# Kernel optimization log

Hardware: AMD Instinct MI355X
Metric: run time of the kernel (lower is better)

## Reference

```python
import jax, jax.numpy as jnp
import numpy as np

IN_C = 64
OUT_C = 64
NUM_RELS = 32
N_NODES = 20000
N_EDGES = 50000


def setup_inputs() -> dict:
    key = jax.random.key(0)
    k1, k2, k3, k4, k5, k6, k7 = jax.random.split(key, 7)
    x = jax.random.normal(k1, (N_NODES, IN_C), dtype=jnp.float32)
    edge_index = jax.random.randint(k2, (2, N_EDGES), 0, N_NODES, dtype=jnp.int64)
    edge_type = jax.random.randint(k3, (N_EDGES,), 0, NUM_RELS, dtype=jnp.int64)
    weight_fwd = jax.random.normal(k4, (NUM_RELS, IN_C * OUT_C), dtype=jnp.float32)
    weight_bwd = jax.random.normal(k5, (NUM_RELS, IN_C * OUT_C), dtype=jnp.float32)
    lin_w = jax.random.normal(k6, (OUT_C, IN_C), dtype=jnp.float32) * (1.0 / np.sqrt(IN_C))
    lin_b = jax.random.normal(k7, (OUT_C,), dtype=jnp.float32) * 0.01
    return {"x": x, "edge_index": edge_index, "edge_type": edge_type,
            "weight_fwd": weight_fwd, "weight_bwd": weight_bwd,
            "lin_w": lin_w, "lin_b": lin_b}


def type_gcn_conv(x, src, dst, edge_type, weight_table):
    # degrees[e] = (# edges sharing src[e]) + 1  (faithful to pairwise-compare count)
    n_nodes = x.shape[0]
    counts = jax.ops.segment_sum(jnp.ones(src.shape[0], jnp.float32), src,
                                 num_segments=n_nodes)
    degrees = counts[src] + 1.0                      # [E]
    w = weight_table[edge_type]                      # [E, in*out] gather
    w = w / (jnp.linalg.norm(w, axis=1, keepdims=True) + 0.01)
    w = w / degrees[:, None]
    w = w.reshape(-1, IN_C, OUT_C)                   # [E, in, out]
    msg = jnp.einsum('ei,eio->eo', x[src], w)        # per-edge small matmul
    return jax.ops.segment_sum(msg, dst, num_segments=n_nodes)  # scatter-add at dst


def reference(x, edge_index, edge_type, weight_fwd, weight_bwd, lin_w, lin_b):
    src, dst = edge_index[0], edge_index[1]
    fwd = type_gcn_conv(x, src, dst, edge_type, weight_fwd)
    # backward conv sees reversed edge_index: its src is original dst
    bwd = type_gcn_conv(x, dst, src, edge_type, weight_bwd)
    return x @ lin_w.T + lin_b + fwd + bwd
```

## Files before the change

kernel.cpp:

```cpp
#include <hip/hip_runtime.h>

#define NREL 32

typedef short short8 __attribute__((ext_vector_type(8)));
typedef float f32x4 __attribute__((ext_vector_type(4)));

__device__ inline unsigned short f2bf(float f) {
    union { float f; unsigned u; } u; u.f = f;
    unsigned r = u.u + 0x7FFF + ((u.u >> 16) & 1);
    return (unsigned short)(r >> 16);
}


__global__ void count_kernel(const int* __restrict__ src, const int* __restrict__ dst,
                             const int* __restrict__ et,
                             float* __restrict__ cntf, float* __restrict__ cntb,
                             int* __restrict__ hist, int E) {
    __shared__ int lh[NREL];
    if (threadIdx.x < NREL) lh[threadIdx.x] = 0;
    __syncthreads();
    int e = blockIdx.x * blockDim.x + threadIdx.x;
    if (e < E) {
        atomicAdd(&cntf[src[e]], 1.0f);
        atomicAdd(&cntb[dst[e]], 1.0f);
        atomicAdd(&lh[et[e]], 1);
    }
    __syncthreads();
    if (threadIdx.x < NREL && lh[threadIdx.x]) atomicAdd(&hist[threadIdx.x], lh[threadIdx.x]);
}

__global__ void norm_kernel(const float* __restrict__ wf, const float* __restrict__ wb,
                            unsigned short* __restrict__ wtb) {
    int rel = blockIdx.x & 31;
    int tab = blockIdx.x >> 5;
    const float* s_ = (tab ? wb : wf) + rel * 4096;
    unsigned short* d_ = wtb + (size_t)blockIdx.x * 4096;
    int tid = threadIdx.x;

    float ssum = 0.f;
    #pragma unroll
    for (int k = 0; k < 16; k += 4) {
        float4 v = *(const float4*)(s_ + tid * 16 + k);
        ssum += v.x * v.x + v.y * v.y + v.z * v.z + v.w * v.w;
    }
    #pragma unroll
    for (int off = 32; off >= 1; off >>= 1) ssum += __shfl_down(ssum, off, 64);

    __shared__ float part[4];
    __shared__ float scale_s;
    if ((tid & 63) == 0) part[tid >> 6] = ssum;
    __syncthreads();
    if (tid == 0) scale_s = 1.0f / (sqrtf(part[0] + part[1] + part[2] + part[3]) + 0.01f);
    __syncthreads();
    float sc = scale_s;
    int i = tid >> 2, o0 = (tid & 3) * 16;
    #pragma unroll
    for (int q = 0; q < 4; ++q) {
        float4 v = *(const float4*)(s_ + i * 64 + o0 + q * 4);
        d_[(o0 + q * 4 + 0) * 64 + i] = f2bf(v.x * sc);
        d_[(o0 + q * 4 + 1) * 64 + i] = f2bf(v.y * sc);
        d_[(o0 + q * 4 + 2) * 64 + i] = f2bf(v.z * sc);
        d_[(o0 + q * 4 + 3) * 64 + i] = f2bf(v.w * sc);
    }
}

__global__ void prefix_kernel(const int* __restrict__ hist, int* __restrict__ bstart,
                              int* __restrict__ cinfo, int maxC) {
    __shared__ int off[NREL + 1];
    int tid = threadIdx.x;
    if (tid == 0) {
        int acc = 0;
        for (int b = 0; b < NREL; ++b) {
            off[b] = acc;
            bstart[b] = acc;
            acc += ((hist[b] + 63) >> 6) << 6;
        }
        off[NREL] = acc;
    }
    __syncthreads();
    for (int c = tid; c < maxC; c += blockDim.x) {
        int pos = c * 64;
        if (pos >= off[NREL]) { cinfo[c] = -1; continue; }
        int lo = 0, hi = NREL;
        while (hi - lo > 1) { int mid = (lo + hi) >> 1; if (off[mid] <= pos) lo = mid; else hi = mid; }
        cinfo[c] = lo;
    }
}

__global__ void scatter_kernel(const int* __restrict__ et, int* __restrict__ fill,
                               const int* __restrict__ bstart, int* __restrict__ sorted, int E) {
    __shared__ int lh[NREL];
    __shared__ int lbase[NREL];
    int tid = threadIdx.x;
    if (tid < NREL) lh[tid] = 0;
    __syncthreads();
    int e = blockIdx.x * blockDim.x + tid;
    int r = 0, my = 0;
    bool valid = (e < E);
    if (valid) { r = et[e]; my = atomicAdd(&lh[r], 1); }
    __syncthreads();
    if (tid < NREL && lh[tid]) lbase[tid] = atomicAdd(&fill[tid], lh[tid]);
    __syncthreads();
    if (valid) sorted[bstart[r] + lbase[r] + my] = e;
}

__global__ void transpose_lw(const float* __restrict__ lw, float* __restrict__ lwT) {
    int t = threadIdx.x;
    for (int k = t * 16; k < t * 16 + 16; ++k) {
        int o = k & 63, i = k >> 6;
        lwT[k] = lw[o * 64 + i];
    }
}

__global__ void linear_kernel(const float* __restrict__ x, const float* __restrict__ lwT,
                              const float* __restrict__ lb, float* __restrict__ out, int N) {
    __shared__ float xs[4][64];
    int lane = threadIdx.x & 63;
    int wslot = threadIdx.x >> 6;
    int n = blockIdx.x * 4 + wslot;
    bool valid = (n < N);
    int nn = valid ? n : 0;
    xs[wslot][lane] = x[nn * 64 + lane];
    __syncthreads();
    float acc = lb[lane];
    #pragma unroll
    for (int i = 0; i < 64; i += 4) {
        float4 xi = *(const float4*)(&xs[wslot][i]);
        acc = fmaf(xi.x, lwT[(i + 0) * 64 + lane], acc);
        acc = fmaf(xi.y, lwT[(i + 1) * 64 + lane], acc);
        acc = fmaf(xi.z, lwT[(i + 2) * 64 + lane], acc);
        acc = fmaf(xi.w, lwT[(i + 3) * 64 + lane], acc);
    }
    if (valid) out[n * 64 + lane] = acc;
}

#define APITCH 72
__global__ __launch_bounds__(256) void conv_mfma(
        const float* __restrict__ x,
        const int* __restrict__ src, const int* __restrict__ dst,
        const float* __restrict__ cntf, const float* __restrict__ cntb,
        const unsigned short* __restrict__ wtb,
        const int* __restrict__ cinfo, const int* __restrict__ sorted,
        float* __restrict__ out) {
    int rel = cinfo[blockIdx.x];
    if (rel < 0) return;
    int dir = blockIdx.y;

    __shared__ unsigned short As[64 * APITCH];
    __shared__ unsigned short Bs[64 * APITCH];
    __shared__ int dstS[64];

    int tid = threadIdx.x;
    int j = tid >> 2, part = tid & 3;

    {
        const uint4* s4 = (const uint4*)(wtb + (size_t)((dir << 5) + rel) * 4096 + j * 64 + part * 16);
        uint4 v0 = s4[0], v1 = s4[1];
        *(uint4*)(&Bs[j * APITCH + part * 16]) = v0;
        *(uint4*)(&Bs[j * APITCH + part * 16 + 8]) = v1;
    }

    int e = sorted[blockIdx.x * 64 + j];
    if (e < 0) {
        uint4 z = {0, 0, 0, 0};
        *(uint4*)(&As[j * APITCH + part * 16]) = z;
        *(uint4*)(&As[j * APITCH + part * 16 + 8]) = z;
        if (part == 0) dstS[j] = -1;
    } else {
        int s_ = dir ? dst[e] : src[e];
        int d_ = dir ? src[e] : dst[e];
        float cv = dir ? cntb[s_] : cntf[s_];
        float inv = 1.0f / (cv + 1.0f);
        const float4* xr = (const float4*)(x + (size_t)s_ * 64 + part * 16);
        float4 v0 = xr[0], v1 = xr[1], v2 = xr[2], v3 = xr[3];
        uint4 r0, r1;
        r0.x = f2bf(v0.x * inv) | ((unsigned)f2bf(v0.y * inv) << 16);
        r0.y = f2bf(v0.z * inv) | ((unsigned)f2bf(v0.w * inv) << 16);
        r0.z = f2bf(v1.x * inv) | ((unsigned)f2bf(v1.y * inv) << 16);
        r0.w = f2bf(v1.z * inv) | ((unsigned)f2bf(v1.w * inv) << 16);
        r1.x = f2bf(v2.x * inv) | ((unsigned)f2bf(v2.y * inv) << 16);
        r1.y = f2bf(v2.z * inv) | ((unsigned)f2bf(v2.w * inv) << 16);
        r1.z = f2bf(v3.x * inv) | ((unsigned)f2bf(v3.y * inv) << 16);
        r1.w = f2bf(v3.z * inv) | ((unsigned)f2bf(v3.w * inv) << 16);
        *(uint4*)(&As[j * APITCH + part * 16]) = r0;
        *(uint4*)(&As[j * APITCH + part * 16 + 8]) = r1;
        if (part == 0) dstS[j] = d_;
    }
    __syncthreads();

    int lane = tid & 63, w = tid >> 6;
    int m = lane & 15, quad = lane >> 4;
    f32x4 acc0 = {0.f, 0.f, 0.f, 0.f}, acc1 = acc0, acc2 = acc0, acc3 = acc0;
    #pragma unroll
    for (int k0 = 0; k0 < 64; k0 += 32) {
        short8 a  = *(const short8*)(&As[(w * 16 + m) * APITCH + k0 + quad * 8]);
        short8 b0 = *(const short8*)(&Bs[(0  + m) * APITCH + k0 + quad * 8]);
        short8 b1 = *(const short8*)(&Bs[(16 + m) * APITCH + k0 + quad * 8]);
        short8 b2 = *(const short8*)(&Bs[(32 + m) * APITCH + k0 + quad * 8]);
        short8 b3 = *(const short8*)(&Bs[(48 + m) * APITCH + k0 + quad * 8]);
        acc0 = __builtin_amdgcn_mfma_f32_16x16x32_bf16(a, b0, acc0, 0, 0, 0);
        acc1 = __builtin_amdgcn_mfma_f32_16x16x32_bf16(a, b1, acc1, 0, 0, 0);
        acc2 = __builtin_amdgcn_mfma_f32_16x16x32_bf16(a, b2, acc2, 0, 0, 0);
        acc3 = __builtin_amdgcn_mfma_f32_16x16x32_bf16(a, b3, acc3, 0, 0, 0);
    }

    int row_base = w * 16 + quad * 4;
    #pragma unroll
    for (int r = 0; r < 4; ++r) {
        int d_ = dstS[row_base + r];
        if (d_ >= 0) {
            float* op = out + (size_t)d_ * 64 + m;
            atomicAdd(op +  0, acc0[r]);
            atomicAdd(op + 16, acc1[r]);
            atomicAdd(op + 32, acc2[r]);
            atomicAdd(op + 48, acc3[r]);
        }
    }
}

extern "C" void kernel_launch(void* const* d_in, const int* in_sizes, int n_in,
                              void* d_out, int out_size, void* d_ws, size_t ws_size,
                              hipStream_t stream) {
    const float* x  = (const float*)d_in[0];
    const int*   ei = (const int*)  d_in[1];
    const int*   et = (const int*)  d_in[2];
    const float* wf = (const float*)d_in[3];
    const float* wb = (const float*)d_in[4];
    const float* lw = (const float*)d_in[5];
    const float* lb = (const float*)d_in[6];
    float* out = (float*)d_out;

    const int E = in_sizes[2];
    const int N = in_sizes[0] / 64;
    const int maxC = ((E + 63) >> 6) + NREL;

    char* p = (char*)d_ws;
    unsigned short* wtb = (unsigned short*)p;  p += (size_t)2 * NREL * 4096 * sizeof(unsigned short);
    float* lwT  = (float*)p;                   p += 4096 * sizeof(float);
    float* cntf = (float*)p;                   p += (size_t)N * sizeof(float);
    float* cntb = (float*)p;                   p += (size_t)N * sizeof(float);
    int*   hist = (int*)p;                     p += NREL * sizeof(int);
    int*   fill = (int*)p;                     p += NREL * sizeof(int);
    int*   bst  = (int*)p;                     p += NREL * sizeof(int);
    int*   cinfo = (int*)p;                    p += (size_t)maxC * sizeof(int);
    int*   sorted = (int*)p;                   p += (size_t)maxC * 64 * sizeof(int);

    const int* srcp = ei;
    const int* dstp = ei + E;

    hipMemsetAsync(cntf, 0, ((size_t)2 * N + 2 * NREL) * sizeof(float), stream);
    hipMemsetAsync(sorted, 0xFF, (size_t)maxC * 64 * sizeof(int), stream);

    count_kernel<<<(E + 255) / 256, 256, 0, stream>>>(srcp, dstp, et, cntf, cntb, hist, E);
    prefix_kernel<<<1, 256, 0, stream>>>(hist, bst, cinfo, maxC);
    scatter_kernel<<<(E + 255) / 256, 256, 0, stream>>>(et, fill, bst, sorted, E);
    norm_kernel<<<64, 256, 0, stream>>>(wf, wb, wtb);
    transpose_lw<<<1, 256, 0, stream>>>(lw, lwT);
    linear_kernel<<<(N + 3) / 4, 256, 0, stream>>>(x, lwT, lb, out, N);
    dim3 cgrid(maxC, 2);
    conv_mfma<<<cgrid, 256, 0, stream>>>(x, srcp, dstp, cntf, cntb, wtb, cinfo, sorted, out);
}
```

Baseline: 134.9 us.

## Fuse setup kernels into one launch and derive bucket offsets on the fly

Measured after the change: 115.2 us. 14.6% less time.

```diff
diff --git a/kernel.cpp b/kernel.cpp
--- a/kernel.cpp
+++ b/kernel.cpp
@@ -11,87 +11,122 @@
     return (unsigned short)(r >> 16);
 }
 
-
-__global__ void count_kernel(const int* __restrict__ src, const int* __restrict__ dst,
-                             const int* __restrict__ et,
-                             float* __restrict__ cntf, float* __restrict__ cntb,
-                             int* __restrict__ hist, int E) {
-    __shared__ int lh[NREL];
-    if (threadIdx.x < NREL) lh[threadIdx.x] = 0;
-    __syncthreads();
-    int e = blockIdx.x * blockDim.x + threadIdx.x;
-    if (e < E) {
-        atomicAdd(&cntf[src[e]], 1.0f);
-        atomicAdd(&cntb[dst[e]], 1.0f);
-        atomicAdd(&lh[et[e]], 1);
-    }
-    __syncthreads();
-    if (threadIdx.x < NREL && lh[threadIdx.x]) atomicAdd(&hist[threadIdx.x], lh[threadIdx.x]);
-}
-
-__global__ void norm_kernel(const float* __restrict__ wf, const float* __restrict__ wb,
-                            unsigned short* __restrict__ wtb) {
-    int rel = blockIdx.x & 31;
-    int tab = blockIdx.x >> 5;
-    const float* s_ = (tab ? wb : wf) + rel * 4096;
-    unsigned short* d_ = wtb + (size_t)blockIdx.x * 4096;
+__device__ inline void bucket_scan(const int* __restrict__ hist, int lane,
+                                   int& h, int& P, int& excl) {
+    h = (lane < NREL) ? hist[lane] : 0;
+    P = ((h + 63) >> 6) << 6;
+    int s = P;
+    #pragma unroll
+    for (int off = 1; off < 32; off <<= 1) {
+        int t = __shfl_up(s, off, 64);
+        if ((lane & 31) >= off) s += t;
+    }
+    excl = s - P;
+}
+
+
+__global__ __launch_bounds__(256) void setup_kernel(
+        const float* __restrict__ x,
+        const int* __restrict__ src, const int* __restrict__ dst,
+        const int* __restrict__ et,
+        const float* __restrict__ wf, const float* __restrict__ wb,
+        const float* __restrict__ lw, const float* __restrict__ lb,
+        float* __restrict__ cntf, float* __restrict__ cntb,
+        int* __restrict__ hist, unsigned short* __restrict__ wtb,
+        float* __restrict__ out, int E, int N, int nCountB) {
+    __shared__ float smem[4 * 8 * 64 + 8];
     int tid = threadIdx.x;
-
-    float ssum = 0.f;
-    #pragma unroll
-    for (int k = 0; k < 16; k += 4) {
-        float4 v = *(const float4*)(s_ + tid * 16 + k);
-        ssum += v.x * v.x + v.y * v.y + v.z * v.z + v.w * v.w;
-    }
-    #pragma unroll
-    for (int off = 32; off >= 1; off >>= 1) ssum += __shfl_down(ssum, off, 64);
-
-    __shared__ float part[4];
-    __shared__ float scale_s;
-    if ((tid & 63) == 0) part[tid >> 6] = ssum;
-    __syncthreads();
-    if (tid == 0) scale_s = 1.0f / (sqrtf(part[0] + part[1] + part[2] + part[3]) + 0.01f);
-    __syncthreads();
-    float sc = scale_s;
-    int i = tid >> 2, o0 = (tid & 3) * 16;
-    #pragma unroll
-    for (int q = 0; q < 4; ++q) {
-        float4 v = *(const float4*)(s_ + i * 64 + o0 + q * 4);
-        d_[(o0 + q * 4 + 0) * 64 + i] = f2bf(v.x * sc);
-        d_[(o0 + q * 4 + 1) * 64 + i] = f2bf(v.y * sc);
-        d_[(o0 + q * 4 + 2) * 64 + i] = f2bf(v.z * sc);
-        d_[(o0 + q * 4 + 3) * 64 + i] = f2bf(v.w * sc);
-    }
-}
-
-__global__ void prefix_kernel(const int* __restrict__ hist, int* __restrict__ bstart,
-                              int* __restrict__ cinfo, int maxC) {
-    __shared__ int off[NREL + 1];
-    int tid = threadIdx.x;
-    if (tid == 0) {
-        int acc = 0;
-        for (int b = 0; b < NREL; ++b) {
-            off[b] = acc;
-            bstart[b] = acc;
-            acc += ((hist[b] + 63) >> 6) << 6;
-        }
-        off[NREL] = acc;
-    }
-    __syncthreads();
-    for (int c = tid; c < maxC; c += blockDim.x) {
-        int pos = c * 64;
-        if (pos >= off[NREL]) { cinfo[c] = -1; continue; }
-        int lo = 0, hi = NREL;
-        while (hi - lo > 1) { int mid = (lo + hi) >> 1; if (off[mid] <= pos) lo = mid; else hi = mid; }
-        cinfo[c] = lo;
+    int b = blockIdx.x;
+
+    if (b < nCountB) {
+        int* lh = (int*)smem;
+        if (tid < NREL) lh[tid] = 0;
+        __syncthreads();
+        int e = b * 256 + tid;
+        if (e < E) {
+            atomicAdd(&cntf[src[e]], 1.0f);
+            atomicAdd(&cntb[dst[e]], 1.0f);
+            atomicAdd(&lh[et[e]], 1);
+        }
+        __syncthreads();
+        if (tid < NREL && lh[tid]) atomicAdd(&hist[tid], lh[tid]);
+        return;
+    }
+    b -= nCountB;
+    if (b < 64) {
+        int rel = b & 31, tab = b >> 5;
+        const float* s_ = (tab ? wb : wf) + rel * 4096;
+        unsigned short* d_ = wtb + (size_t)b * 4096;
+        float* part = smem;
+        float ssum = 0.f;
+        #pragma unroll
+        for (int k = 0; k < 16; k += 4) {
+            float4 v = *(const float4*)(s_ + tid * 16 + k);
+            ssum += v.x * v.x + v.y * v.y + v.z * v.z + v.w * v.w;
+        }
+        #pragma unroll
+        for (int off = 32; off >= 1; off >>= 1) ssum += __shfl_down(ssum, off, 64);
+        if ((tid & 63) == 0) part[tid >> 6] = ssum;
+        __syncthreads();
+        if (tid == 0) part[4] = 1.0f / (sqrtf(part[0] + part[1] + part[2] + part[3]) + 0.01f);
+        __syncthreads();
+        float sc = part[4];
+        int i = tid >> 2, o0 = (tid & 3) * 16;
+        #pragma unroll
+        for (int q = 0; q < 4; ++q) {
+            float4 v = *(const float4*)(s_ + i * 64 + o0 + q * 4);
+            d_[(o0 + q * 4 + 0) * 64 + i] = f2bf(v.x * sc);
+            d_[(o0 + q * 4 + 1) * 64 + i] = f2bf(v.y * sc);
+            d_[(o0 + q * 4 + 2) * 64 + i] = f2bf(v.z * sc);
+            d_[(o0 + q * 4 + 3) * 64 + i] = f2bf(v.w * sc);
+        }
+        return;
+    }
+    b -= 64;
+    {
+        int lane = tid & 63, w = tid >> 6;
+        int nodeBase = b * 32 + w * 8;
+        float4 wrow[16];
+        const float4* lwrow = (const float4*)(lw + lane * 64);
+        #pragma unroll
+        for (int g = 0; g < 16; ++g) wrow[g] = lwrow[g];
+        float bias = lb[lane];
+        float* xs = smem + w * 8 * 64;
+        #pragma unroll
+        for (int t = 0; t < 8; ++t) {
+            int n = nodeBase + t;
+            if (n < N) xs[t * 64 + lane] = x[(size_t)n * 64 + lane];
+        }
+        __syncthreads();
+        for (int t = 0; t < 8; ++t) {
+            int n = nodeBase + t;
+            if (n >= N) break;
+            float acc = bias;
+            const float4* xr = (const float4*)(xs + t * 64);
+            #pragma unroll
+            for (int g = 0; g < 16; ++g) {
+                float4 xv = xr[g];
+                acc = fmaf(xv.x, wrow[g].x, acc);
+                acc = fmaf(xv.y, wrow[g].y, acc);
+                acc = fmaf(xv.z, wrow[g].z, acc);
+                acc = fmaf(xv.w, wrow[g].w, acc);
+            }
+            out[(size_t)n * 64 + lane] = acc;
+        }
     }
 }
 
 __global__ void scatter_kernel(const int* __restrict__ et, int* __restrict__ fill,
-                               const int* __restrict__ bstart, int* __restrict__ sorted, int E) {
+                               const int* __restrict__ hist, int* __restrict__ sorted, int E) {
     __shared__ int lh[NREL];
     __shared__ int lbase[NREL];
+    __shared__ int bstartS[NREL];
     int tid = threadIdx.x;
+    if (tid < 64) {
+        int h, P, excl;
+        bucket_scan(hist, tid, h, P, excl);
+        if (tid < NREL) bstartS[tid] = excl;
+    }
     if (tid < NREL) lh[tid] = 0;
     __syncthreads();
     int e = blockIdx.x * blockDim.x + tid;
@@ -101,37 +136,7 @@
     __syncthreads();
     if (tid < NREL && lh[tid]) lbase[tid] = atomicAdd(&fill[tid], lh[tid]);
     __syncthreads();
-    if (valid) sorted[bstart[r] + lbase[r] + my] = e;
-}
-
-__global__ void transpose_lw(const float* __restrict__ lw, float* __restrict__ lwT) {
-    int t = threadIdx.x;
-    for (int k = t * 16; k < t * 16 + 16; ++k) {
-        int o = k & 63, i = k >> 6;
-        lwT[k] = lw[o * 64 + i];
-    }
-}
-
-__global__ void linear_kernel(const float* __restrict__ x, const float* __restrict__ lwT,
-                              const float* __restrict__ lb, float* __restrict__ out, int N) {
-    __shared__ float xs[4][64];
-    int lane = threadIdx.x & 63;
-    int wslot = threadIdx.x >> 6;
-    int n = blockIdx.x * 4 + wslot;
-    bool valid = (n < N);
-    int nn = valid ? n : 0;
-    xs[wslot][lane] = x[nn * 64 + lane];
-    __syncthreads();
-    float acc = lb[lane];
-    #pragma unroll
-    for (int i = 0; i < 64; i += 4) {
-        float4 xi = *(const float4*)(&xs[wslot][i]);
-        acc = fmaf(xi.x, lwT[(i + 0) * 64 + lane], acc);
-        acc = fmaf(xi.y, lwT[(i + 1) * 64 + lane], acc);
-        acc = fmaf(xi.z, lwT[(i + 2) * 64 + lane], acc);
-        acc = fmaf(xi.w, lwT[(i + 3) * 64 + lane], acc);
-    }
-    if (valid) out[n * 64 + lane] = acc;
+    if (valid) sorted[bstartS[r] + lbase[r] + my] = e;
 }
 
 #define APITCH 72
@@ -139,18 +144,28 @@
         const float* __restrict__ x,
         const int* __restrict__ src, const int* __restrict__ dst,
         const float* __restrict__ cntf, const float* __restrict__ cntb,
+        const int* __restrict__ hist,
         const unsigned short* __restrict__ wtb,
-        const int* __restrict__ cinfo, const int* __restrict__ sorted,
+        const int* __restrict__ sorted,
         float* __restrict__ out) {
-    int rel = cinfo[blockIdx.x];
-    if (rel < 0) return;
+    int tid = threadIdx.x;
+    int lane = tid & 63;
+    int h, P, excl;
+    bucket_scan(hist, lane, h, P, excl);
+    int pos = blockIdx.x * 64;
+    unsigned long long m_ = __ballot(lane < NREL && pos >= excl && pos < excl + P);
+    if (m_ == 0) return;
+    int rel = __ffsll(m_) - 1;
+    int start = __shfl(excl, rel, 64);
+    int hr = __shfl(h, rel, 64);
+    int valid = hr - (pos - start);
+    if (valid > 64) valid = 64;
     int dir = blockIdx.y;
 
     __shared__ unsigned short As[64 * APITCH];
     __shared__ unsigned short Bs[64 * APITCH];
     __shared__ int dstS[64];
 
-    int tid = threadIdx.x;
     int j = tid >> 2, part = tid & 3;
 
     {
@@ -160,13 +175,13 @@
         *(uint4*)(&Bs[j * APITCH + part * 16 + 8]) = v1;
     }
 
-    int e = sorted[blockIdx.x * 64 + j];
-    if (e < 0) {
+    if (j >= valid) {
         uint4 z = {0, 0, 0, 0};
         *(uint4*)(&As[j * APITCH + part * 16]) = z;
         *(uint4*)(&As[j * APITCH + part * 16 + 8]) = z;
         if (part == 0) dstS[j] = -1;
     } else {
+        int e = sorted[pos + j];
         int s_ = dir ? dst[e] : src[e];
         int d_ = dir ? src[e] : dst[e];
         float cv = dir ? cntb[s_] : cntf[s_];
@@ -188,7 +203,7 @@
     }
     __syncthreads();
 
-    int lane = tid & 63, w = tid >> 6;
+    int w = tid >> 6;
     int m = lane & 15, quad = lane >> 4;
     f32x4 acc0 = {0.f, 0.f, 0.f, 0.f}, acc1 = acc0, acc2 = acc0, acc3 = acc0;
     #pragma unroll
@@ -236,27 +251,22 @@
 
     char* p = (char*)d_ws;
     unsigned short* wtb = (unsigned short*)p;  p += (size_t)2 * NREL * 4096 * sizeof(unsigned short);
-    float* lwT  = (float*)p;                   p += 4096 * sizeof(float);
     float* cntf = (float*)p;                   p += (size_t)N * sizeof(float);
     float* cntb = (float*)p;                   p += (size_t)N * sizeof(float);
     int*   hist = (int*)p;                     p += NREL * sizeof(int);
     int*   fill = (int*)p;                     p += NREL * sizeof(int);
-    int*   bst  = (int*)p;                     p += NREL * sizeof(int);
-    int*   cinfo = (int*)p;                    p += (size_t)maxC * sizeof(int);
     int*   sorted = (int*)p;                   p += (size_t)maxC * 64 * sizeof(int);
 
     const int* srcp = ei;
     const int* dstp = ei + E;
 
     hipMemsetAsync(cntf, 0, ((size_t)2 * N + 2 * NREL) * sizeof(float), stream);
-    hipMemsetAsync(sorted, 0xFF, (size_t)maxC * 64 * sizeof(int), stream);
-
-    count_kernel<<<(E + 255) / 256, 256, 0, stream>>>(srcp, dstp, et, cntf, cntb, hist, E);
-    prefix_kernel<<<1, 256, 0, stream>>>(hist, bst, cinfo, maxC);
-    scatter_kernel<<<(E + 255) / 256, 256, 0, stream>>>(et, fill, bst, sorted, E);
-    norm_kernel<<<64, 256, 0, stream>>>(wf, wb, wtb);
-    transpose_lw<<<1, 256, 0, stream>>>(lw, lwT);
-    linear_kernel<<<(N + 3) / 4, 256, 0, stream>>>(x, lwT, lb, out, N);
+
+    const int nCountB = (E + 255) / 256;
+    const int nLinB   = (N + 31) / 32;
+    setup_kernel<<<nCountB + 64 + nLinB, 256, 0, stream>>>(
+        x, srcp, dstp, et, wf, wb, lw, lb, cntf, cntb, hist, wtb, out, E, N, nCountB);
+    scatter_kernel<<<(E + 255) / 256, 256, 0, stream>>>(et, fill, hist, sorted, E);
     dim3 cgrid(maxC, 2);
-    conv_mfma<<<cgrid, 256, 0, stream>>>(x, srcp, dstp, cntf, cntb, wtb, cinfo, sorted, out);
-}
+    conv_mfma<<<cgrid, 256, 0, stream>>>(x, srcp, dstp, cntf, cntb, hist, wtb, sorted, out);
+}
```
